# Kernel optimization log

Hardware: AMD Instinct MI355X
Metric: run time of the kernel (lower is better)

Reference implementation:

```python
import jax, jax.numpy as jnp
import numpy as np

NEIGHBORS = 9
GROUP = 8
EPS = 1e-5


def grid_sample_border(feat, grid):
    """Bilinear grid_sample, padding_mode='border', align_corners=False.
    feat: [B,C,H,W], grid: [B,Hg,Wg,2] in [-1,1] -> [B,C,Hg,Wg]."""
    B, C, H, W = feat.shape
    gx, gy = grid[..., 0], grid[..., 1]
    # unnormalize (align_corners=False) then clip to border
    ix = jnp.clip(((gx + 1.0) * W - 1.0) * 0.5, 0.0, W - 1.0)
    iy = jnp.clip(((gy + 1.0) * H - 1.0) * 0.5, 0.0, H - 1.0)
    x0 = jnp.floor(ix)
    y0 = jnp.floor(iy)
    wx = ix - x0  # [B,Hg,Wg]
    wy = iy - y0
    x0i = x0.astype(jnp.int32)
    y0i = y0.astype(jnp.int32)
    x1i = jnp.minimum(x0i + 1, W - 1)
    y1i = jnp.minimum(y0i + 1, H - 1)

    def sample_one(f, y0i, x0i, y1i, x1i, wx, wy):  # f [C,H,W]
        v00 = f[:, y0i, x0i]  # [C,Hg,Wg]
        v01 = f[:, y0i, x1i]
        v10 = f[:, y1i, x0i]
        v11 = f[:, y1i, x1i]
        return (v00 * (1 - wx) * (1 - wy) + v01 * wx * (1 - wy)
                + v10 * (1 - wx) * wy + v11 * wx * wy)

    return jax.vmap(sample_one)(feat, y0i, x0i, y1i, x1i, wx, wy)


def bn_relu(x, gamma, beta, mean, var):  # channel axis 1
    shp = (1, -1, 1, 1, 1)
    inv = gamma.reshape(shp) * jax.lax.rsqrt(var.reshape(shp) + EPS)
    return jax.nn.relu((x - mean.reshape(shp)) * inv + beta.reshape(shp))


def setup_inputs() -> dict:
    key = jax.random.key(0)
    ks = jax.random.split(key, 8)
    B, C, H, W = 4, 64, 128, 160
    ref_feature = jax.random.normal(ks[0], (B, C, H, W), dtype=jnp.float32)
    grid = jax.random.uniform(ks[1], (B, NEIGHBORS * H, W, 2), dtype=jnp.float32) * 2.0 - 1.0
    return {
        "ref_feature": ref_feature,
        "grid": grid,
        "w0": jax.random.normal(ks[2], (16, GROUP), dtype=jnp.float32) * 0.1,
        "g0": jnp.ones((16,), jnp.float32), "b0": jnp.zeros((16,), jnp.float32),
        "m0": jnp.zeros((16,), jnp.float32), "v0": jnp.ones((16,), jnp.float32),
        "w1": jax.random.normal(ks[3], (8, 16), dtype=jnp.float32) * 0.1,
        "g1": jnp.ones((8,), jnp.float32), "b1": jnp.zeros((8,), jnp.float32),
        "m1": jnp.zeros((8,), jnp.float32), "v1": jnp.ones((8,), jnp.float32),
        "w_sim": jax.random.normal(ks[4], (1, 8), dtype=jnp.float32) * 0.1,
        "b_sim": jnp.zeros((1,), jnp.float32),
    }


def reference(ref_feature, grid, w0, g0, b0, m0, v0, w1, g1, b1, m1, v1, w_sim, b_sim):
    B, C, H, W = ref_feature.shape
    G = GROUP
    N = NEIGHBORS
    sampled = grid_sample_border(ref_feature, grid)  # [B,C,N*H,W]
    weight = sampled.reshape(B, G, C // G, N, H, W)
    ref = ref_feature.reshape(B, G, C // G, 1, H, W)
    weight = (weight * ref).mean(axis=2)  # [B,G,N,H,W]
    # 1x1x1 conv stacks == channel matmuls
    x = bn_relu(jnp.einsum('og,bgnhw->bonhw', w0, weight), g0, b0, m0, v0)
    x = bn_relu(jnp.einsum('oc,bcnhw->bonhw', w1, x), g1, b1, m1, v1)
    x = jnp.einsum('oc,bcnhw->bonhw', w_sim, x) + b_sim.reshape(1, -1, 1, 1, 1)
    return jax.nn.sigmoid(x).squeeze(1)  # [B,N,H,W]
```

## Files before the change

### kernel.cpp

```cpp
#include <hip/hip_runtime.h>
#include <hip/hip_bf16.h>
#include <hip/hip_fp16.h>

#define B_   4
#define C_   64
#define H_   128
#define W_   160
#define N_   9
#define HW_  (H_*W_)
#define NPTS (B_*N_*H_*W_)
#define EPS_ 1e-5f

#define TFEAT_BYTES (B_*HW_*C_*2)

typedef _Float16 h2_t __attribute__((ext_vector_type(2)));
union U4 { uint4 u; h2_t h[4]; };

__global__ __launch_bounds__(256) void transpose_fuse(
    const float* __restrict__ feat,
    const float* __restrict__ w0, const float* __restrict__ g0, const float* __restrict__ b0,
    const float* __restrict__ m0, const float* __restrict__ v0,
    const float* __restrict__ w1, const float* __restrict__ g1, const float* __restrict__ b1,
    const float* __restrict__ m1, const float* __restrict__ v1,
    const float* __restrict__ wsim, const float* __restrict__ bsim,
    _Float16* __restrict__ tf, float* __restrict__ fw)
{
    __shared__ float tile[64][65];
    const int blk = blockIdx.x;
    const int bi  = blk / 320;
    const int hw0 = (blk - bi * 320) * 64;
    const int t   = threadIdx.x;
    const int lhw = t & 63;
    const int cq  = t >> 6;

    const float* fb = feat + (size_t)bi * C_ * HW_;
    #pragma unroll
    for (int k = 0; k < 16; ++k) {
        int c = cq * 16 + k;
        tile[c][lhw] = fb[c * HW_ + hw0 + lhw];
    }
    __syncthreads();
    const int c_out = t & 63;
    #pragma unroll
    for (int k = 0; k < 16; ++k) {
        int hw = cq * 16 + k;
        tf[((size_t)bi * HW_ + hw0 + hw) * C_ + c_out] =
            (_Float16)tile[c_out][hw];
    }

    if (blk == 0) {
        if (t < 16) {
            float inv = g0[t] * rsqrtf(v0[t] + EPS_);
            for (int g = 0; g < 8; ++g) fw[t * 8 + g] = w0[t * 8 + g] * inv;
            fw[128 + t] = b0[t] - m0[t] * inv;
        } else if (t < 24) {
            int o = t - 16;
            float inv = g1[o] * rsqrtf(v1[o] + EPS_);
            for (int c = 0; c < 16; ++c) fw[144 + o * 16 + c] = w1[o * 16 + c] * inv;
            fw[272 + o] = b1[o] - m1[o] * inv;
        } else if (t == 24) {
            for (int c = 0; c < 8; ++c) fw[280 + c] = wsim[c];
            fw[288] = bsim[0];
        }
    }
}

__global__ __launch_bounds__(256) void fwnet_main(
    const float* __restrict__ grid, const _Float16* __restrict__ tf,
    const float* __restrict__ fw, float* __restrict__ out)
{
    __shared__ float wlds[256 * 8];

    const int t   = threadIdx.x;
    const int bid = blockIdx.x;
    const int sb    = (bid & 7) * (2880 / 8) + (bid >> 3);
    const int pbase = sb * 256;
    const int j     = t & 7;

    #pragma unroll 2
    for (int r = 0; r < 8; ++r) {
        const int q = r * 32 + (t >> 3);
        const int p = pbase + q;

        const int px  = p % W_;
        const int row = p / W_;
        const int bn  = row / H_;
        const int h   = row - bn * H_;
        const int bi  = bn / N_;

        const float2 gv = ((const float2*)grid)[p];
        float ix = fminf(fmaxf(((gv.x + 1.0f) * (float)W_ - 1.0f) * 0.5f, 0.0f), (float)(W_ - 1));
        float iy = fminf(fmaxf(((gv.y + 1.0f) * (float)H_ - 1.0f) * 0.5f, 0.0f), (float)(H_ - 1));
        float x0f = floorf(ix), y0f = floorf(iy);
        float wx = ix - x0f, wy = iy - y0f;
        int x0 = (int)x0f, y0 = (int)y0f;
        int x1 = min(x0 + 1, W_ - 1), y1 = min(y0 + 1, H_ - 1);
        float w00 = (1.0f - wx) * (1.0f - wy);
        float w01 = wx * (1.0f - wy);
        float w10 = (1.0f - wx) * wy;
        float w11 = wx * wy;

        const _Float16* Tb = tf + (size_t)bi * (HW_ * C_);
        U4 a, b2, c2, d2, rr;
        a.u  = *((const uint4*)(Tb + (y0 * W_ + x0) * C_) + j);
        b2.u = *((const uint4*)(Tb + (y0 * W_ + x1) * C_) + j);
        c2.u = *((const uint4*)(Tb + (y1 * W_ + x0) * C_) + j);
        d2.u = *((const uint4*)(Tb + (y1 * W_ + x1) * C_) + j);
        rr.u = *((const uint4*)(Tb + (h  * W_ + px) * C_) + j);

        float d00 = 0.f, d01 = 0.f, d10 = 0.f, d11 = 0.f;
        #pragma unroll
        for (int k = 0; k < 4; ++k) {
#if __has_builtin(__builtin_amdgcn_fdot2)
            d00 = __builtin_amdgcn_fdot2(a.h[k],  rr.h[k], d00, false);
            d01 = __builtin_amdgcn_fdot2(b2.h[k], rr.h[k], d01, false);
            d10 = __builtin_amdgcn_fdot2(c2.h[k], rr.h[k], d10, false);
            d11 = __builtin_amdgcn_fdot2(d2.h[k], rr.h[k], d11, false);
#else
            d00 = fmaf((float)a.h[k].x,  (float)rr.h[k].x, fmaf((float)a.h[k].y,  (float)rr.h[k].y, d00));
            d01 = fmaf((float)b2.h[k].x, (float)rr.h[k].x, fmaf((float)b2.h[k].y, (float)rr.h[k].y, d01));
            d10 = fmaf((float)c2.h[k].x, (float)rr.h[k].x, fmaf((float)c2.h[k].y, (float)rr.h[k].y, d10));
            d11 = fmaf((float)d2.h[k].x, (float)rr.h[k].x, fmaf((float)d2.h[k].y, (float)rr.h[k].y, d11));
#endif
        }
        wlds[q * 8 + j] = (w00 * d00 + w01 * d01 + w10 * d10 + w11 * d11) * 0.125f;
    }
    __syncthreads();

    float wv[8];
    {
        const float4 lo = ((const float4*)wlds)[t * 2];
        const float4 hi = ((const float4*)wlds)[t * 2 + 1];
        wv[0] = lo.x; wv[1] = lo.y; wv[2] = lo.z; wv[3] = lo.w;
        wv[4] = hi.x; wv[5] = hi.y; wv[6] = hi.z; wv[7] = hi.w;
    }

    float h0[16];
    #pragma unroll
    for (int o = 0; o < 16; ++o) {
        float acc = fw[128 + o];
        #pragma unroll
        for (int g = 0; g < 8; ++g) acc = fmaf(fw[o * 8 + g], wv[g], acc);
        h0[o] = fmaxf(acc, 0.0f);
    }
    float h1[8];
    #pragma unroll
    for (int o = 0; o < 8; ++o) {
        float acc = fw[272 + o];
        #pragma unroll
        for (int c = 0; c < 16; ++c) acc = fmaf(fw[144 + o * 16 + c], h0[c], acc);
        h1[o] = fmaxf(acc, 0.0f);
    }
    float s = fw[288];
    #pragma unroll
    for (int c = 0; c < 8; ++c) s = fmaf(fw[280 + c], h1[c], s);

    out[pbase + t] = 1.0f / (1.0f + __expf(-s));
}

extern "C" void kernel_launch(void* const* d_in, const int* in_sizes, int n_in,
                              void* d_out, int out_size, void* d_ws, size_t ws_size,
                              hipStream_t stream) {
    const float* feat = (const float*)d_in[0];
    const float* grid = (const float*)d_in[1];
    const float* w0   = (const float*)d_in[2];
    const float* g0   = (const float*)d_in[3];
    const float* b0   = (const float*)d_in[4];
    const float* m0   = (const float*)d_in[5];
    const float* v0   = (const float*)d_in[6];
    const float* w1   = (const float*)d_in[7];
    const float* g1   = (const float*)d_in[8];
    const float* b1   = (const float*)d_in[9];
    const float* m1   = (const float*)d_in[10];
    const float* v1   = (const float*)d_in[11];
    const float* wsim = (const float*)d_in[12];
    const float* bsim = (const float*)d_in[13];

    _Float16* tf = (_Float16*)d_ws;
    float* fw = (float*)((char*)d_ws + TFEAT_BYTES);

    hipLaunchKernelGGL(transpose_fuse, dim3(B_ * (HW_ / 64)), dim3(256), 0, stream,
                       feat, w0, g0, b0, m0, v0, w1, g1, b1, m1, v1, wsim, bsim, tf, fw);

    hipLaunchKernelGGL(fwnet_main, dim3(NPTS / 256), dim3(256), 0, stream,
                       grid, tf, fw, (float*)d_out);
}
```

Baseline: 41.81 us.

## Precompute per-point sample records in LDS and vectorize transpose stores

Each thread now computes grid coordinates, bilinear offsets and weights once per point and stores them in an LDS record. Previously every one of the eight lanes sharing a point recomputed them. The gather loop reads these records and uses byte offsets directly, and the bilinear blend becomes a lerp form. The transpose kernel now writes four fp16 channels per 8-byte store instead of scalar 2-byte stores, trading more strided LDS reads for fewer, wider global writes. The extra LDS buffer and barrier add some overhead.

New measurement: 36.30 us. 1.15x faster.

```diff
diff --git a/kernel.cpp b/kernel.cpp
--- a/kernel.cpp
+++ b/kernel.cpp
@@ -10,11 +10,13 @@
 #define HW_  (H_*W_)
 #define NPTS (B_*N_*H_*W_)
 #define EPS_ 1e-5f
+#define ROWB (C_*2)
 
 #define TFEAT_BYTES (B_*HW_*C_*2)
 
 typedef _Float16 h2_t __attribute__((ext_vector_type(2)));
 union U4 { uint4 u; h2_t h[4]; };
+union H2U { h2_t h; unsigned u; };
 
 __global__ __launch_bounds__(256) void transpose_fuse(
     const float* __restrict__ feat,
@@ -40,12 +42,16 @@
         tile[c][lhw] = fb[c * HW_ + hw0 + lhw];
     }
     __syncthreads();
-    const int c_out = t & 63;
-    #pragma unroll
-    for (int k = 0; k < 16; ++k) {
-        int hw = cq * 16 + k;
-        tf[((size_t)bi * HW_ + hw0 + hw) * C_ + c_out] =
-            (_Float16)tile[c_out][hw];
+
+    const int c4 = (t & 15) * 4;
+    #pragma unroll
+    for (int k = 0; k < 4; ++k) {
+        int hw = k * 16 + (t >> 4);
+        H2U lo, hi;
+        lo.h = h2_t{ (_Float16)tile[c4 + 0][hw], (_Float16)tile[c4 + 1][hw] };
+        hi.h = h2_t{ (_Float16)tile[c4 + 2][hw], (_Float16)tile[c4 + 3][hw] };
+        uint2 val; val.x = lo.u; val.y = hi.u;
+        *(uint2*)(tf + ((size_t)bi * HW_ + hw0 + hw) * C_ + c4) = val;
     }
 
     if (blk == 0) {
@@ -70,18 +76,15 @@
     const float* __restrict__ fw, float* __restrict__ out)
 {
     __shared__ float wlds[256 * 8];
+    __shared__ int   rec[256 * 8];
 
     const int t   = threadIdx.x;
     const int bid = blockIdx.x;
     const int sb    = (bid & 7) * (2880 / 8) + (bid >> 3);
     const int pbase = sb * 256;
-    const int j     = t & 7;
-
-    #pragma unroll 2
-    for (int r = 0; r < 8; ++r) {
-        const int q = r * 32 + (t >> 3);
-        const int p = pbase + q;
-
+
+    {
+        const int p   = pbase + t;
         const int px  = p % W_;
         const int row = p / W_;
         const int bn  = row / H_;
@@ -95,18 +98,39 @@
         float wx = ix - x0f, wy = iy - y0f;
         int x0 = (int)x0f, y0 = (int)y0f;
         int x1 = min(x0 + 1, W_ - 1), y1 = min(y0 + 1, H_ - 1);
-        float w00 = (1.0f - wx) * (1.0f - wy);
-        float w01 = wx * (1.0f - wy);
-        float w10 = (1.0f - wx) * wy;
-        float w11 = wx * wy;
-
-        const _Float16* Tb = tf + (size_t)bi * (HW_ * C_);
+
+        const int ib = bi * HW_;
+        int4 rA, rB;
+        rA.x = __float_as_int(wx);
+        rA.y = __float_as_int(wy);
+        rA.z = (ib + y0 * W_ + x0) * ROWB;
+        rA.w = (ib + y0 * W_ + x1) * ROWB;
+        rB.x = (ib + y1 * W_ + x0) * ROWB;
+        rB.y = (ib + y1 * W_ + x1) * ROWB;
+        rB.z = (ib + h  * W_ + px) * ROWB;
+        rB.w = 0;
+        ((int4*)rec)[t * 2]     = rA;
+        ((int4*)rec)[t * 2 + 1] = rB;
+    }
+    __syncthreads();
+
+    const int j = t & 7;
+    const char* base = (const char*)tf;
+    #pragma unroll 2
+    for (int r = 0; r < 8; ++r) {
+        const int q = r * 32 + (t >> 3);
+        const int4 rA = ((const int4*)rec)[q * 2];
+        const int4 rB = ((const int4*)rec)[q * 2 + 1];
+        const float wx = __int_as_float(rA.x);
+        const float wy = __int_as_float(rA.y);
+        const int jo = j * 16;
+
         U4 a, b2, c2, d2, rr;
-        a.u  = *((const uint4*)(Tb + (y0 * W_ + x0) * C_) + j);
-        b2.u = *((const uint4*)(Tb + (y0 * W_ + x1) * C_) + j);
-        c2.u = *((const uint4*)(Tb + (y1 * W_ + x0) * C_) + j);
-        d2.u = *((const uint4*)(Tb + (y1 * W_ + x1) * C_) + j);
-        rr.u = *((const uint4*)(Tb + (h  * W_ + px) * C_) + j);
+        a.u  = *(const uint4*)(base + rA.z + jo);
+        b2.u = *(const uint4*)(base + rA.w + jo);
+        c2.u = *(const uint4*)(base + rB.x + jo);
+        d2.u = *(const uint4*)(base + rB.y + jo);
+        rr.u = *(const uint4*)(base + rB.z + jo);
 
         float d00 = 0.f, d01 = 0.f, d10 = 0.f, d11 = 0.f;
         #pragma unroll
@@ -123,7 +147,9 @@
             d11 = fmaf((float)d2.h[k].x, (float)rr.h[k].x, fmaf((float)d2.h[k].y, (float)rr.h[k].y, d11));
 #endif
         }
-        wlds[q * 8 + j] = (w00 * d00 + w01 * d01 + w10 * d10 + w11 * d11) * 0.125f;
+        float dy0 = d00 + wx * (d01 - d00);
+        float dy1 = d10 + wx * (d11 - d10);
+        wlds[q * 8 + j] = (dy0 + wy * (dy1 - dy0)) * 0.125f;
     }
     __syncthreads();
 
```
